# Kernel tuning notes

Measured on AMD Instinct MI355X. Metric: run time of the kernel, lower is better.

## Reference

```python
import jax, jax.numpy as jnp
import numpy as np

N, H, M, B = 64, 64, 32, 16384
relu = jax.nn.relu


def setup_inputs() -> dict:
    key = jax.random.key(0)
    ks = jax.random.split(key, 10)
    s = 0.05
    x = jax.random.normal(ks[0], (B, N), dtype=jnp.float32)
    # stacked per-node weights (torch Linear applies x @ W.T, W: [out, in])
    W1a = jax.random.normal(ks[1], (N, H, N), dtype=jnp.float32) * s   # directed net layer 1
    W1b = jax.random.normal(ks[2], (N, M, H), dtype=jnp.float32) * s   # directed net layer 2
    W2a = jax.random.normal(ks[3], (N, H, N), dtype=jnp.float32) * s   # bi-directed net layer 1
    W2b = jax.random.normal(ks[4], (N, M, H), dtype=jnp.float32) * s   # bi-directed net layer 2
    W3a = jax.random.normal(ks[5], (N, H, 2 * M + N), dtype=jnp.float32) * s  # fuse layer 1
    b3a = jax.random.normal(ks[6], (N, H), dtype=jnp.float32) * s
    W3b = jax.random.normal(ks[7], (N, 1, H), dtype=jnp.float32) * s          # fuse layer 2
    b3b = jax.random.normal(ks[8], (N, 1), dtype=jnp.float32) * s
    return {"x": x, "W1a": W1a, "W1b": W1b, "W2a": W2a, "W2b": W2b,
            "W3a": W3a, "b3a": b3a, "W3b": W3b, "b3b": b3b}


def reference(x, W1a, W1b, W2a, W2b, W3a, b3a, W3b, b3b):
    Bsz, n = x.shape
    eye = jnp.eye(n, dtype=x.dtype)
    off = 1.0 - eye  # filter_1; adjacency at init is also (ones - eye), so mask is idempotent
    # inputs_1_dag / inputs_1_bi: [B, N, N] per-node masked copies of x
    x1 = jnp.einsum('bn,in->bin', x, off)
    # inputs_2: [B, N, N] with x[b,i] on the diagonal of row i
    x2 = eye[None, :, :] * x[:, None, :]
    # directed branch: ReLU(Linear) -> ReLU(Linear), batched over node i
    r1 = relu(jnp.einsum('bih,imh->bim', relu(jnp.einsum('bin,ihn->bih', x1, W1a)), W1b))
    # bi-directed branch (same masked input at init)
    r2 = relu(jnp.einsum('bih,imh->bim', relu(jnp.einsum('bin,ihn->bih', x1, W2a)), W2b))
    feat = jnp.concatenate([r1, r2, x2], axis=2)  # [B, N, 2M+N]
    h = relu(jnp.einsum('bik,ihk->bih', feat, W3a) + b3a[None])
    out = relu(jnp.einsum('bih,ioh->bio', h, W3b) + b3b[None])  # [B, N, 1]
    return out[..., 0]  # [B, N] causal derivative
```

## Files before the change

### kernel.cpp

```cpp
#include <hip/hip_runtime.h>


typedef short bf16x8 __attribute__((ext_vector_type(8)));
typedef float f32x4  __attribute__((ext_vector_type(4)));
typedef unsigned int u32x4 __attribute__((ext_vector_type(4)));

__device__ __forceinline__ unsigned int pack2(float a, float b) {
    union { float f; unsigned int u; } ua, ub; ua.f = a; ub.f = b;
    return __builtin_amdgcn_perm(ub.u + 0x8000u, ua.u + 0x8000u, 0x07060302u);
}

__device__ __forceinline__ f32x4 mfma16(bf16x8 a, bf16x8 b, f32x4 c) {
    return __builtin_amdgcn_mfma_f32_16x16x32_bf16(a, b, c, 0, 0, 0);
}

__device__ __forceinline__ bf16x8 pack_frag(f32x4 lo, f32x4 hi) {
    union { u32x4 u; bf16x8 v; } r;
    r.u[0] = pack2(fmaxf(lo[0], 0.f), fmaxf(lo[1], 0.f));
    r.u[1] = pack2(fmaxf(lo[2], 0.f), fmaxf(lo[3], 0.f));
    r.u[2] = pack2(fmaxf(hi[0], 0.f), fmaxf(hi[1], 0.f));
    r.u[3] = pack2(fmaxf(hi[2], 0.f), fmaxf(hi[3], 0.f));
    return r.v;
}

__device__ __forceinline__ bf16x8 cvt_frag2(const float* __restrict__ plo,
                                            const float* __restrict__ phi) {
    f32x4 f0 = *(const f32x4*)plo;
    f32x4 f1 = *(const f32x4*)phi;
    union { u32x4 u; bf16x8 v; } r;
    r.u[0] = pack2(f0[0], f0[1]);
    r.u[1] = pack2(f0[2], f0[3]);
    r.u[2] = pack2(f1[0], f1[1]);
    r.u[3] = pack2(f1[2], f1[3]);
    return r.v;
}

__device__ __forceinline__ bf16x8 cvt_frag2_m(const float* __restrict__ plo,
                                              const float* __restrict__ phi,
                                              const unsigned int* M) {
    f32x4 f0 = *(const f32x4*)plo;
    f32x4 f1 = *(const f32x4*)phi;
    union { u32x4 u; bf16x8 v; } r;
    r.u[0] = pack2(f0[0], f0[1]) & M[0];
    r.u[1] = pack2(f0[2], f0[3]) & M[1];
    r.u[2] = pack2(f1[0], f1[1]) & M[2];
    r.u[3] = pack2(f1[2], f1[3]) & M[3];
    return r.v;
}

__global__ __launch_bounds__(256) void prep_x(const float* __restrict__ x,
                                              unsigned short* __restrict__ xb) {
    int j = (blockIdx.x * 256 + threadIdx.x) * 8;
    f32x4 a = *(const f32x4*)&x[j];
    f32x4 b = *(const f32x4*)&x[j + 4];
    u32x4 r = { pack2(a[0], a[1]), pack2(a[2], a[3]), pack2(b[0], b[1]), pack2(b[2], b[3]) };
    *(u32x4*)&xb[j] = r;
}

__global__ __launch_bounds__(256, 2) void main_kernel(
    const float* __restrict__ x,
    const float* __restrict__ W1a, const float* __restrict__ W1b,
    const float* __restrict__ W2a, const float* __restrict__ W2b,
    const float* __restrict__ W3a, const float* __restrict__ b3a,
    const float* __restrict__ W3b, const float* __restrict__ b3b,
    const unsigned short* __restrict__ xb,
    float* __restrict__ out)
{
    const int i    = blockIdx.x & 63;
    const int bg   = blockIdx.x >> 6;
    const int tid  = threadIdx.x;
    const int w    = tid >> 6;
    const int lane = tid & 63;
    const int q    = lane >> 4;
    const int c0   = lane & 15;

    unsigned int M[2][4];
    {
        const unsigned int halfmask = (i & 1) ? 0x0000FFFFu : 0xFFFF0000u;
        const int dz = (i >> 1) & 3;
        #pragma unroll
        for (int s = 0; s < 2; ++s) {
            bool hit = ((i >> 3) == s * 4 + q);
            #pragma unroll
            for (int d = 0; d < 4; ++d)
                M[s][d] = (hit && d == dz) ? halfmask : 0xFFFFFFFFu;
        }
    }

    bf16x8 A1[4][2], A2[4][2];
    {
        const float* p1 = W1a + (i << 12);
        const float* p2 = W2a + (i << 12);
        #pragma unroll
        for (int t = 0; t < 4; ++t)
            #pragma unroll
            for (int s = 0; s < 2; ++s) {
                int off = (((t << 4) + c0) << 6) + (s << 5) + (q << 3);
                A1[t][s] = cvt_frag2_m(p1 + off, p1 + off + 4, M[s]);
                A2[t][s] = cvt_frag2_m(p2 + off, p2 + off + 4, M[s]);
            }
    }
    bf16x8 F1[2][2], F2[2][2];
    {
        const float* p1 = W1b + (i << 11);
        const float* p2 = W2b + (i << 11);
        #pragma unroll
        for (int t = 0; t < 2; ++t)
            #pragma unroll
            for (int s = 0; s < 2; ++s) {
                int base = (((t << 4) + c0) << 6) + (s << 5) + (q << 2);
                F1[t][s] = cvt_frag2(p1 + base, p1 + base + 16);
                F2[t][s] = cvt_frag2(p2 + base, p2 + base + 16);
            }
    }
    bf16x8 A3[4][2];
    {
        const float* p3 = W3a + (i << 13);
        #pragma unroll
        for (int t = 0; t < 4; ++t)
            #pragma unroll
            for (int s = 0; s < 2; ++s) {
                int base = (((t << 4) + c0) << 7) + (s << 5) + (q << 2);
                A3[t][s] = cvt_frag2(p3 + base, p3 + base + 16);
            }
    }
    f32x4 b3av[4], w3xv[4], w3bv[4];
    #pragma unroll
    for (int t = 0; t < 4; ++t) {
        int h0 = (i << 6) + (t << 4) + (q << 2);
        b3av[t] = *(const f32x4*)&b3a[h0];
        w3bv[t] = *(const f32x4*)&W3b[h0];
        #pragma unroll
        for (int r = 0; r < 4; ++r)
            w3xv[t][r] = W3a[(i << 13) + (((t << 4) + (q << 2) + r) << 7) + 64 + i];
    }
    const float bb = b3b[i];

    const int rbase0 = (((bg << 2) + w) << 9);

    int row = rbase0 + c0;
    bf16x8 XB0 = *(const bf16x8*)&xb[(row << 6) + (q << 3)];
    bf16x8 XB1 = *(const bf16x8*)&xb[(row << 6) + 32 + (q << 3)];
    float   xd = x[(row << 6) + i];

    for (int k = 0; k < 32; ++k) {
        int nrow = rbase0 + ((k < 31 ? k + 1 : 31) << 4) + c0;
        bf16x8 nXB0 = *(const bf16x8*)&xb[(nrow << 6) + (q << 3)];
        bf16x8 nXB1 = *(const bf16x8*)&xb[(nrow << 6) + 32 + (q << 3)];
        float   nxd = x[(nrow << 6) + i];

        f32x4 a1[4], a2[4];
        #pragma unroll
        for (int t = 0; t < 4; ++t) {
            f32x4 z = {0.f, 0.f, 0.f, 0.f};
            f32x4 u = mfma16(A1[t][0], XB0, z);
            a1[t]   = mfma16(A1[t][1], XB1, u);
            f32x4 v = mfma16(A2[t][0], XB0, z);
            a2[t]   = mfma16(A2[t][1], XB1, v);
        }
        bf16x8 HB0 = pack_frag(a1[0], a1[1]);
        bf16x8 HB1 = pack_frag(a1[2], a1[3]);
        bf16x8 GB0 = pack_frag(a2[0], a2[1]);
        bf16x8 GB1 = pack_frag(a2[2], a2[3]);

        f32x4 b1[2], b2[2];
        #pragma unroll
        for (int t = 0; t < 2; ++t) {
            f32x4 z = {0.f, 0.f, 0.f, 0.f};
            f32x4 u = mfma16(F1[t][0], HB0, z);
            b1[t]   = mfma16(F1[t][1], HB1, u);
            f32x4 v = mfma16(F2[t][0], GB0, z);
            b2[t]   = mfma16(F2[t][1], GB1, v);
        }
        bf16x8 RB0 = pack_frag(b1[0], b1[1]);
        bf16x8 RB1 = pack_frag(b2[0], b2[1]);

        float p = 0.f;
        #pragma unroll
        for (int t = 0; t < 4; ++t) {
            f32x4 acc;
            #pragma unroll
            for (int r = 0; r < 4; ++r) acc[r] = fmaf(xd, w3xv[t][r], b3av[t][r]);
            acc = mfma16(A3[t][0], RB0, acc);
            acc = mfma16(A3[t][1], RB1, acc);
            #pragma unroll
            for (int r = 0; r < 4; ++r) p = fmaf(fmaxf(acc[r], 0.f), w3bv[t][r], p);
        }
        p += __shfl_xor(p, 16);
        p += __shfl_xor(p, 32);
        if (lane < 16) out[(row << 6) + i] = fmaxf(p + bb, 0.f);

        row = nrow; XB0 = nXB0; XB1 = nXB1; xd = nxd;
    }
}

extern "C" void kernel_launch(void* const* d_in, const int* in_sizes, int n_in,
                              void* d_out, int out_size, void* d_ws, size_t ws_size,
                              hipStream_t stream) {
    (void)in_sizes; (void)n_in; (void)out_size; (void)ws_size;
    const float* x   = (const float*)d_in[0];
    const float* W1a = (const float*)d_in[1];
    const float* W1b = (const float*)d_in[2];
    const float* W2a = (const float*)d_in[3];
    const float* W2b = (const float*)d_in[4];
    const float* W3a = (const float*)d_in[5];
    const float* b3a = (const float*)d_in[6];
    const float* W3b = (const float*)d_in[7];
    const float* b3b = (const float*)d_in[8];
    float* out = (float*)d_out;
    unsigned short* xb = (unsigned short*)d_ws;

    prep_x<<<512, 256, 0, stream>>>(x, xb);
    main_kernel<<<512, 256, 0, stream>>>(x, W1a, W1b, W2a, W2b, W3a, b3a, W3b, b3b, xb, out);
}
```

Measured before the change: 131.0 us.

## Stage weight fragments in LDS cooperatively and process two row tiles per iteration

Per-node weight fragments used to be converted and held in registers by every wave. Now each wave converts a disjoint subset once and writes it to shared memory, and the bias and W3 vectors are staged there too. The main loop handles two 16-row tiles per iteration, so each LDS fragment read feeds two MFMAs and there is more independent MFMA work to interleave. The aim is to cut redundant global weight loads and register pressure, at the cost of LDS reads inside the loop, a block barrier and roughly 33KB of LDS per block, which may limit occupancy.

```diff
diff --git a/kernel.cpp b/kernel.cpp
--- a/kernel.cpp
+++ b/kernel.cpp
@@ -74,6 +74,9 @@
     const int q    = lane >> 4;
     const int c0   = lane & 15;
 
+    __shared__ short lfrag[32 * 512];
+    __shared__ float s_vec[3][4][4][4];
+
     unsigned int M[2][4];
     {
         const unsigned int halfmask = (i & 1) ? 0x0000FFFFu : 0xFFFF0000u;
@@ -87,110 +90,151 @@
         }
     }
 
-    bf16x8 A1[4][2], A2[4][2];
-    {
+    if (w == 0) {
         const float* p1 = W1a + (i << 12);
+        #pragma unroll
+        for (int j = 0; j < 8; ++j) {
+            int t = j >> 1, s = j & 1;
+            int off = (((t << 4) + c0) << 6) + (s << 5) + (q << 3);
+            bf16x8 fr = cvt_frag2_m(p1 + off, p1 + off + 4, M[s]);
+            *(bf16x8*)&lfrag[j * 512 + lane * 8] = fr;
+        }
+    } else if (w == 1) {
         const float* p2 = W2a + (i << 12);
         #pragma unroll
-        for (int t = 0; t < 4; ++t)
-            #pragma unroll
-            for (int s = 0; s < 2; ++s) {
-                int off = (((t << 4) + c0) << 6) + (s << 5) + (q << 3);
-                A1[t][s] = cvt_frag2_m(p1 + off, p1 + off + 4, M[s]);
-                A2[t][s] = cvt_frag2_m(p2 + off, p2 + off + 4, M[s]);
+        for (int j = 0; j < 8; ++j) {
+            int t = j >> 1, s = j & 1;
+            int off = (((t << 4) + c0) << 6) + (s << 5) + (q << 3);
+            bf16x8 fr = cvt_frag2_m(p2 + off, p2 + off + 4, M[s]);
+            *(bf16x8*)&lfrag[(8 + j) * 512 + lane * 8] = fr;
+        }
+    } else if (w == 2) {
+        const float* p3 = W3a + (i << 13);
+        #pragma unroll
+        for (int j = 0; j < 8; ++j) {
+            int t = j >> 1, s = j & 1;
+            int base = (((t << 4) + c0) << 7) + (s << 5) + (q << 2);
+            bf16x8 fr = cvt_frag2(p3 + base, p3 + base + 16);
+            *(bf16x8*)&lfrag[(16 + j) * 512 + lane * 8] = fr;
+        }
+    } else {
+        const float* pb1 = W1b + (i << 11);
+        const float* pb2 = W2b + (i << 11);
+        #pragma unroll
+        for (int j = 0; j < 4; ++j) {
+            int t = j >> 1, s = j & 1;
+            int base = (((t << 4) + c0) << 6) + (s << 5) + (q << 2);
+            bf16x8 fr1 = cvt_frag2(pb1 + base, pb1 + base + 16);
+            bf16x8 fr2 = cvt_frag2(pb2 + base, pb2 + base + 16);
+            *(bf16x8*)&lfrag[(24 + j) * 512 + lane * 8] = fr1;
+            *(bf16x8*)&lfrag[(28 + j) * 512 + lane * 8] = fr2;
+        }
+    }
+    if (tid < 64) {
+        int tt = tid >> 4, qq = (tid >> 2) & 3, rr = tid & 3;
+        s_vec[0][tt][qq][rr] = b3a[(i << 6) + tid];
+        s_vec[2][tt][qq][rr] = W3b[(i << 6) + tid];
+        s_vec[1][tt][qq][rr] = W3a[(i << 13) + (tid << 7) + 64 + i];
+    }
+    const float bb = b3b[i];
+    __syncthreads();
+
+    const int wbase = (((bg << 2) + w) << 9);
+
+    bf16x8 XB0[2], XB1[2]; float xd[2];
+    #pragma unroll
+    for (int r = 0; r < 2; ++r) {
+        int rw = wbase + (r << 4) + c0;
+        XB0[r] = *(const bf16x8*)&xb[(rw << 6) + (q << 3)];
+        XB1[r] = *(const bf16x8*)&xb[(rw << 6) + 32 + (q << 3)];
+        xd[r]  = x[(rw << 6) + i];
+    }
+
+    for (int k = 0; k < 16; ++k) {
+        int nb = wbase + ((k < 15 ? k + 1 : 15) << 5) + c0;
+        bf16x8 nXB0[2], nXB1[2]; float nxd[2];
+        #pragma unroll
+        for (int r = 0; r < 2; ++r) {
+            int rw = nb + (r << 4);
+            nXB0[r] = *(const bf16x8*)&xb[(rw << 6) + (q << 3)];
+            nXB1[r] = *(const bf16x8*)&xb[(rw << 6) + 32 + (q << 3)];
+            nxd[r]  = x[(rw << 6) + i];
+        }
+
+        f32x4 a1[4][2], a2[4][2];
+        #pragma unroll
+        for (int t = 0; t < 4; ++t) {
+            bf16x8 f10 = *(const bf16x8*)&lfrag[(t * 2 + 0) * 512 + lane * 8];
+            bf16x8 f11 = *(const bf16x8*)&lfrag[(t * 2 + 1) * 512 + lane * 8];
+            bf16x8 f20 = *(const bf16x8*)&lfrag[(8 + t * 2 + 0) * 512 + lane * 8];
+            bf16x8 f21 = *(const bf16x8*)&lfrag[(8 + t * 2 + 1) * 512 + lane * 8];
+            #pragma unroll
+            for (int r = 0; r < 2; ++r) {
+                f32x4 z = {0.f, 0.f, 0.f, 0.f};
+                a1[t][r] = mfma16(f11, XB1[r], mfma16(f10, XB0[r], z));
+                a2[t][r] = mfma16(f21, XB1[r], mfma16(f20, XB0[r], z));
             }
-    }
-    bf16x8 F1[2][2], F2[2][2];
-    {
-        const float* p1 = W1b + (i << 11);
-        const float* p2 = W2b + (i << 11);
-        #pragma unroll
-        for (int t = 0; t < 2; ++t)
-            #pragma unroll
-            for (int s = 0; s < 2; ++s) {
-                int base = (((t << 4) + c0) << 6) + (s << 5) + (q << 2);
-                F1[t][s] = cvt_frag2(p1 + base, p1 + base + 16);
-                F2[t][s] = cvt_frag2(p2 + base, p2 + base + 16);
+        }
+        bf16x8 HB0[2], HB1[2], GB0[2], GB1[2];
+        #pragma unroll
+        for (int r = 0; r < 2; ++r) {
+            HB0[r] = pack_frag(a1[0][r], a1[1][r]);
+            HB1[r] = pack_frag(a1[2][r], a1[3][r]);
+            GB0[r] = pack_frag(a2[0][r], a2[1][r]);
+            GB1[r] = pack_frag(a2[2][r], a2[3][r]);
+        }
+
+        f32x4 b1[2][2], b2[2][2];
+        #pragma unroll
+        for (int t = 0; t < 2; ++t) {
+            bf16x8 g10 = *(const bf16x8*)&lfrag[(24 + t * 2 + 0) * 512 + lane * 8];
+            bf16x8 g11 = *(const bf16x8*)&lfrag[(24 + t * 2 + 1) * 512 + lane * 8];
+            bf16x8 g20 = *(const bf16x8*)&lfrag[(28 + t * 2 + 0) * 512 + lane * 8];
+            bf16x8 g21 = *(const bf16x8*)&lfrag[(28 + t * 2 + 1) * 512 + lane * 8];
+            #pragma unroll
+            for (int r = 0; r < 2; ++r) {
+                f32x4 z = {0.f, 0.f, 0.f, 0.f};
+                b1[t][r] = mfma16(g11, HB1[r], mfma16(g10, HB0[r], z));
+                b2[t][r] = mfma16(g21, GB1[r], mfma16(g20, GB0[r], z));
             }
-    }
-    bf16x8 A3[4][2];
-    {
-        const float* p3 = W3a + (i << 13);
-        #pragma unroll
-        for (int t = 0; t < 4; ++t)
-            #pragma unroll
-            for (int s = 0; s < 2; ++s) {
-                int base = (((t << 4) + c0) << 7) + (s << 5) + (q << 2);
-                A3[t][s] = cvt_frag2(p3 + base, p3 + base + 16);
+        }
+        bf16x8 RB0[2], RB1[2];
+        #pragma unroll
+        for (int r = 0; r < 2; ++r) {
+            RB0[r] = pack_frag(b1[0][r], b1[1][r]);
+            RB1[r] = pack_frag(b2[0][r], b2[1][r]);
+        }
+
+        float p[2] = {0.f, 0.f};
+        #pragma unroll
+        for (int t = 0; t < 4; ++t) {
+            bf16x8 h0 = *(const bf16x8*)&lfrag[(16 + t * 2 + 0) * 512 + lane * 8];
+            bf16x8 h1 = *(const bf16x8*)&lfrag[(16 + t * 2 + 1) * 512 + lane * 8];
+            f32x4 bv = *(const f32x4*)&s_vec[0][t][q][0];
+            f32x4 xv = *(const f32x4*)&s_vec[1][t][q][0];
+            f32x4 wv = *(const f32x4*)&s_vec[2][t][q][0];
+            #pragma unroll
+            for (int r = 0; r < 2; ++r) {
+                f32x4 acc;
+                #pragma unroll
+                for (int e = 0; e < 4; ++e) acc[e] = fmaf(xd[r], xv[e], bv[e]);
+                acc = mfma16(h0, RB0[r], acc);
+                acc = mfma16(h1, RB1[r], acc);
+                #pragma unroll
+                for (int e = 0; e < 4; ++e) p[r] = fmaf(fmaxf(acc[e], 0.f), wv[e], p[r]);
             }
-    }
-    f32x4 b3av[4], w3xv[4], w3bv[4];
-    #pragma unroll
-    for (int t = 0; t < 4; ++t) {
-        int h0 = (i << 6) + (t << 4) + (q << 2);
-        b3av[t] = *(const f32x4*)&b3a[h0];
-        w3bv[t] = *(const f32x4*)&W3b[h0];
-        #pragma unroll
-        for (int r = 0; r < 4; ++r)
-            w3xv[t][r] = W3a[(i << 13) + (((t << 4) + (q << 2) + r) << 7) + 64 + i];
-    }
-    const float bb = b3b[i];
-
-    const int rbase0 = (((bg << 2) + w) << 9);
-
-    int row = rbase0 + c0;
-    bf16x8 XB0 = *(const bf16x8*)&xb[(row << 6) + (q << 3)];
-    bf16x8 XB1 = *(const bf16x8*)&xb[(row << 6) + 32 + (q << 3)];
-    float   xd = x[(row << 6) + i];
-
-    for (int k = 0; k < 32; ++k) {
-        int nrow = rbase0 + ((k < 31 ? k + 1 : 31) << 4) + c0;
-        bf16x8 nXB0 = *(const bf16x8*)&xb[(nrow << 6) + (q << 3)];
-        bf16x8 nXB1 = *(const bf16x8*)&xb[(nrow << 6) + 32 + (q << 3)];
-        float   nxd = x[(nrow << 6) + i];
-
-        f32x4 a1[4], a2[4];
-        #pragma unroll
-        for (int t = 0; t < 4; ++t) {
-            f32x4 z = {0.f, 0.f, 0.f, 0.f};
-            f32x4 u = mfma16(A1[t][0], XB0, z);
-            a1[t]   = mfma16(A1[t][1], XB1, u);
-            f32x4 v = mfma16(A2[t][0], XB0, z);
-            a2[t]   = mfma16(A2[t][1], XB1, v);
-        }
-        bf16x8 HB0 = pack_frag(a1[0], a1[1]);
-        bf16x8 HB1 = pack_frag(a1[2], a1[3]);
-        bf16x8 GB0 = pack_frag(a2[0], a2[1]);
-        bf16x8 GB1 = pack_frag(a2[2], a2[3]);
-
-        f32x4 b1[2], b2[2];
-        #pragma unroll
-        for (int t = 0; t < 2; ++t) {
-            f32x4 z = {0.f, 0.f, 0.f, 0.f};
-            f32x4 u = mfma16(F1[t][0], HB0, z);
-            b1[t]   = mfma16(F1[t][1], HB1, u);
-            f32x4 v = mfma16(F2[t][0], GB0, z);
-            b2[t]   = mfma16(F2[t][1], GB1, v);
-        }
-        bf16x8 RB0 = pack_frag(b1[0], b1[1]);
-        bf16x8 RB1 = pack_frag(b2[0], b2[1]);
-
-        float p = 0.f;
-        #pragma unroll
-        for (int t = 0; t < 4; ++t) {
-            f32x4 acc;
-            #pragma unroll
-            for (int r = 0; r < 4; ++r) acc[r] = fmaf(xd, w3xv[t][r], b3av[t][r]);
-            acc = mfma16(A3[t][0], RB0, acc);
-            acc = mfma16(A3[t][1], RB1, acc);
-            #pragma unroll
-            for (int r = 0; r < 4; ++r) p = fmaf(fmaxf(acc[r], 0.f), w3bv[t][r], p);
-        }
-        p += __shfl_xor(p, 16);
-        p += __shfl_xor(p, 32);
-        if (lane < 16) out[(row << 6) + i] = fmaxf(p + bb, 0.f);
-
-        row = nrow; XB0 = nXB0; XB1 = nXB1; xd = nxd;
+        }
+        #pragma unroll
+        for (int r = 0; r < 2; ++r) {
+            float pp = p[r];
+            pp += __shfl_xor(pp, 16);
+            pp += __shfl_xor(pp, 32);
+            int rw = wbase + (k << 5) + (r << 4) + c0;
+            if (lane < 16) out[(rw << 6) + i] = fmaxf(pp + bb, 0.f);
+        }
+
+        #pragma unroll
+        for (int r = 0; r < 2; ++r) { XB0[r] = nXB0[r]; XB1[r] = nXB1[r]; xd[r] = nxd[r]; }
     }
 }
 
```

New measurement: 121.5 us. -7.3%, faster.
